# Performance work log

Measured on AMD Instinct MI355X. Metric: run time of the kernel, lower is better.

## Reference

```python
import jax, jax.numpy as jnp
import numpy as np

D = 768        # embed_dim
P = 16         # patch_size
DEPTH = 12
FF = 3072      # dim_feedforward = 4*D
NUM_CLASSES = 100
EPS = 1e-5     # nn.LayerNorm default


def _ln(x, g, b):
    m = jnp.mean(x, axis=-1, keepdims=True)
    v = jnp.mean((x - m) ** 2, axis=-1, keepdims=True)
    return (x - m) / jnp.sqrt(v + EPS) * g + b


def setup_inputs() -> dict:
    key = jax.random.key(0)
    ks = jax.random.split(key, 24)
    f32 = jnp.float32
    inp = {
        'x': jax.random.normal(ks[0], (32, 3, 224, 224), dtype=f32),
        # patch embed conv: [C_in, P, P, D] layout for einsum
        'patch_w': jax.random.normal(ks[1], (3, P, P, D), dtype=f32) * 0.02,
        'patch_b': jnp.zeros((D,), f32),
        'cls_token': jax.random.normal(ks[2], (1, 1, D), dtype=f32) * 0.02,
        'pos_embed': jax.random.normal(ks[3], (1, 197, D), dtype=f32) * 0.02,
        # stacked per-layer params; Linear stored as [in, out]
        'Wq': jax.random.normal(ks[4], (DEPTH, D, D), dtype=f32) * 0.02,
        'bq': jnp.zeros((DEPTH, D), f32),
        'Wk': jax.random.normal(ks[5], (DEPTH, D, D), dtype=f32) * 0.02,
        'bk': jnp.zeros((DEPTH, D), f32),
        'Wv': jax.random.normal(ks[6], (DEPTH, D, D), dtype=f32) * 0.02,
        'bv': jnp.zeros((DEPTH, D), f32),
        'W1': jax.random.normal(ks[7], (DEPTH, D, FF), dtype=f32) * 0.02,
        'b1': jnp.zeros((DEPTH, FF), f32),
        'W2': jax.random.normal(ks[8], (DEPTH, FF, D), dtype=f32) * 0.02,
        'b2': jnp.zeros((DEPTH, D), f32),
        'ln1_g': jnp.ones((DEPTH, D), f32),
        'ln1_b': jnp.zeros((DEPTH, D), f32),
        'ln2_g': jnp.ones((DEPTH, D), f32),
        'ln2_b': jnp.zeros((DEPTH, D), f32),
        'lnf_g': jnp.ones((D,), f32),
        'lnf_b': jnp.zeros((D,), f32),
        'head_w': jax.random.normal(ks[9], (D, NUM_CLASSES), dtype=f32) * 0.02,
        'head_b': jnp.zeros((NUM_CLASSES,), f32),
    }
    return inp


def reference(x, patch_w, patch_b, cls_token, pos_embed,
              Wq, bq, Wk, bk, Wv, bv, W1, b1, W2, b2,
              ln1_g, ln1_b, ln2_g, ln2_b, lnf_g, lnf_b,
              head_w, head_b):
    B = x.shape[0]
    Hp = x.shape[2] // P  # 14
    # patch embed: Conv2d(k=16, s=16) == non-overlapping patch projection
    xp = x.reshape(B, 3, Hp, P, Hp, P)
    tok = jnp.einsum('bchpwq,cpqd->bhwd', xp, patch_w).reshape(B, Hp * Hp, D) + patch_b
    tok = jnp.concatenate([jnp.broadcast_to(cls_token, (B, 1, D)), tok], axis=1)
    tok = tok + pos_embed  # [B, 197, D]
    N = tok.shape[1]
    # gumbel noise for F.gumbel_softmax(tau=1, hard=False), one sample per layer
    gnoise = jax.random.gumbel(jax.random.key(1), (DEPTH, B, N, N), dtype=tok.dtype)
    inv_sqrt_d = 1.0 / jnp.sqrt(jnp.asarray(D, tok.dtype))

    def step(src, p):
        (wq, bq_, wk, bk_, wv, bv_, w1, b1_, w2, b2_,
         g1, be1, g2, be2, gn) = p
        Q = src @ wq + bq_
        K = src @ wk + bk_
        V = src @ wv + bv_
        scores = jnp.einsum('bnd,bmd->bnm', Q, K) * inv_sqrt_d
        attn = jax.nn.softmax(scores + gn, axis=-1) @ V
        src = _ln(src + attn, g1, be1)          # note: out_linear unused in source
        ff = jax.nn.gelu(src @ w1 + b1_, approximate=False) @ w2 + b2_
        src = _ln(src + ff, g2, be2)
        return src, None

    xs = (Wq, bq, Wk, bk, Wv, bv, W1, b1, W2, b2,
          ln1_g, ln1_b, ln2_g, ln2_b, gnoise)
    tok, _ = jax.lax.scan(step, tok, xs)
    tok = _ln(tok, lnf_g, lnf_b)
    cls = tok[:, 0]
    return cls @ head_w + head_b
```

## Files before the change

### kernel.cpp

```cpp
#include <hip/hip_runtime.h>
#include <hip/hip_bf16.h>
#include <math.h>


namespace {
constexpr int DIM    = 768;
constexpr int FF_DIM = 3072;
constexpr int QKVN   = 2304;
constexpr int NTOK   = 197;
constexpr int NBATCH = 32;
constexpr int NLAYER = 12;
constexpr int ROWS   = NBATCH * NTOK;
constexpr int NPATCH = 196;
constexpr int PROWS  = NBATCH * NPATCH;
constexpr int KVPAD  = 256;
constexpr float LN_EPS = 1e-5f;
}

typedef __attribute__((ext_vector_type(8))) __bf16 bf16x8;
typedef __attribute__((ext_vector_type(4))) float  f32x4;

__device__ __forceinline__ unsigned rotl32(unsigned v, int d) {
  return (v << d) | (v >> (32 - d));
}

__device__ __forceinline__ float gumbel_noise(unsigned idx) {
  const unsigned ks0 = 0u, ks1 = 1u, ks2 = 0x1BD11BDBu;
  unsigned x0 = 0u + ks0;
  unsigned x1 = idx + ks1;
#define TFR(r) { x0 += x1; x1 = rotl32(x1, (r)); x1 ^= x0; }
  TFR(13) TFR(15) TFR(26) TFR(6)   x0 += ks1; x1 += ks2 + 1u;
  TFR(17) TFR(29) TFR(16) TFR(24)  x0 += ks2; x1 += ks0 + 2u;
  TFR(13) TFR(15) TFR(26) TFR(6)   x0 += ks0; x1 += ks1 + 3u;
  TFR(17) TFR(29) TFR(16) TFR(24)  x0 += ks1; x1 += ks2 + 4u;
  TFR(13) TFR(15) TFR(26) TFR(6)   x0 += ks2; x1 += ks0 + 5u;
#undef TFR
  unsigned bits = x0 ^ x1;
  float f = __uint_as_float((bits >> 9) | 0x3f800000u) - 1.0f;
  const float tiny = 1.17549435e-38f;
  float u = fmaxf(tiny, f + tiny);
  return -logf(-logf(u));
}

__device__ __forceinline__ float block_reduce_sum(float val, float* red) {
  int tid = threadIdx.x;
  red[tid] = val; __syncthreads();
  for (int off = 128; off > 0; off >>= 1) {
    if (tid < off) red[tid] += red[tid + off];
    __syncthreads();
  }
  float r = red[0];
  __syncthreads();
  return r;
}

__device__ __forceinline__ float block_reduce_max(float val, float* red) {
  int tid = threadIdx.x;
  red[tid] = val; __syncthreads();
  for (int off = 128; off > 0; off >>= 1) {
    if (tid < off) red[tid] = fmaxf(red[tid], red[tid + off]);
    __syncthreads();
  }
  float r = red[0];
  __syncthreads();
  return r;
}

__device__ __forceinline__ void async_copy16(const void* g, void* l) {
  __builtin_amdgcn_global_load_lds(
      (const __attribute__((address_space(1))) unsigned*)g,
      (__attribute__((address_space(3))) unsigned*)l, 16, 0, 0);
}

__device__ __forceinline__ int xcd_swizzle(int id, int nwg) {
  const int q = nwg >> 3, r = nwg & 7;
  const int xcd = id & 7, pos = id >> 3;
  return (xcd < r ? xcd * (q + 1) : r * (q + 1) + (xcd - r) * q) + pos;
}

template<int STORE, bool GELU>
__global__ void mm_nt(
    const __hip_bfloat16* __restrict__ A, long sA, int lda,
    const __hip_bfloat16* __restrict__ B, long sB, int ldb,
    void* __restrict__ Cv, long sC, int ldc,
    int M, int N, int K, const float* __restrict__ bias) {
  __shared__ __hip_bfloat16 As[128 * 64];
  __shared__ __hip_bfloat16 Bs[128 * 64];
  const int bz = blockIdx.y;
  A += (long)bz * sA;
  B += (long)bz * sB;
  const int tilesN = (N + 127) >> 7;
  const int id = xcd_swizzle(blockIdx.x, gridDim.x);
  const int row0 = (id / tilesN) * 128, col0 = (id % tilesN) * 128;

  const int tid = threadIdx.x, lane = tid & 63, wid = tid >> 6;
  const int wr = (wid >> 1) * 64, wc = (wid & 1) * 64;
  const int fr = lane & 15;
  const int kh = lane >> 4;
  const int fsw = fr & 7;
  f32x4 acc[4][4] = {};

  const int elem = wid * 512 + lane * 8;

  for (int k0 = 0; k0 < K; k0 += 64) {
    #pragma unroll
    for (int c = 0; c < 4; c++) {
      const int e = c * 2048 + elem;
      const int r = e >> 6;
      const int slot = (e >> 3) & 7;
      const int ksw = ((slot ^ (r & 7)) << 3);
      async_copy16(A + (long)(row0 + r) * lda + k0 + ksw,
                   (char*)As + c * 4096 + wid * 1024);
    }
    #pragma unroll
    for (int c = 0; c < 4; c++) {
      const int e = c * 2048 + elem;
      const int r = e >> 6;
      const int slot = (e >> 3) & 7;
      const int ksw = ((slot ^ (r & 7)) << 3);
      async_copy16(B + (long)(col0 + r) * ldb + k0 + ksw,
                   (char*)Bs + c * 4096 + wid * 1024);
    }
    __syncthreads();
    #pragma unroll
    for (int ks = 0; ks < 2; ks++) {
      bf16x8 a[4], b[4];
      #pragma unroll
      for (int i = 0; i < 4; i++) {
        const int row = wr + i * 16 + fr;
        const int sl  = ((ks << 2) | kh) ^ fsw;
        a[i] = *(const bf16x8*)((const char*)As + row * 128 + (sl << 4));
      }
      #pragma unroll
      for (int j = 0; j < 4; j++) {
        const int row = wc + j * 16 + fr;
        const int sl  = ((ks << 2) | kh) ^ fsw;
        b[j] = *(const bf16x8*)((const char*)Bs + row * 128 + (sl << 4));
      }
      #pragma unroll
      for (int i = 0; i < 4; i++)
        #pragma unroll
        for (int j = 0; j < 4; j++)
          acc[i][j] = __builtin_amdgcn_mfma_f32_16x16x32_bf16(
              a[i], b[j], acc[i][j], 0, 0, 0);
    }
    __syncthreads();
  }

  #pragma unroll
  for (int i = 0; i < 4; i++) {
    #pragma unroll
    for (int j = 0; j < 4; j++) {
      #pragma unroll
      for (int t = 0; t < 4; t++) {
        const int r  = row0 + wr + i * 16 + kh * 4 + t;
        const int cc = col0 + wc + j * 16 + fr;
        if (r < M && cc < N) {
          float v = acc[i][j][t];
          if (bias) v += bias[cc];
          if (GELU) v = 0.5f * v * (1.0f + erff(v * 0.70710678118654752f));
          if (STORE == 0)
            ((float*)Cv)[(long)bz * sC + (long)r * ldc + cc] = v;
          else
            ((__hip_bfloat16*)Cv)[(long)bz * sC + (long)r * ldc + cc] =
                __float2bfloat16(v);
        }
      }
    }
  }
}

__global__ void transpose_bf16_kernel(const float* __restrict__ W,
                                      __hip_bfloat16* __restrict__ Wt,
                                      int K, int N) {
  __shared__ float t[32][33];
  const int k0 = blockIdx.x * 32, n0 = blockIdx.y * 32;
  const int tx = threadIdx.x & 31, ty = threadIdx.x >> 5;
  #pragma unroll
  for (int i = 0; i < 32; i += 8)
    t[ty + i][tx] = W[(long)(k0 + ty + i) * N + n0 + tx];
  __syncthreads();
  #pragma unroll
  for (int i = 0; i < 32; i += 8)
    Wt[(long)(n0 + ty + i) * K + k0 + tx] = __float2bfloat16(t[tx][ty + i]);
}

__global__ void wtrans_kernel(const float* __restrict__ Wq,
                              const float* __restrict__ Wk,
                              const float* __restrict__ Wv,
                              const float* __restrict__ W1,
                              const float* __restrict__ W2,
                              __hip_bfloat16* __restrict__ wqkv_t,
                              __hip_bfloat16* __restrict__ w1_t,
                              __hip_bfloat16* __restrict__ w2_t,
                              long sq, long s1, long s2) {
  __shared__ float t[64][65];
  const int l = blockIdx.y;
  Wq += (long)l * DIM * DIM;  Wk += (long)l * DIM * DIM;
  Wv += (long)l * DIM * DIM;
  W1 += (long)l * DIM * FF_DIM;  W2 += (long)l * FF_DIM * DIM;
  wqkv_t += (long)l * sq;  w1_t += (long)l * s1;  w2_t += (long)l * s2;

  const int id = blockIdx.x;
  const float* W; __hip_bfloat16* O; int K, N, k0, n0;
  if (id < 432) {
    const int m = id / 144, tt = id % 144;
    W = (m == 0) ? Wq : (m == 1) ? Wk : Wv;
    O = wqkv_t + (long)m * DIM * DIM;
    K = DIM; N = DIM; k0 = (tt / 12) * 64; n0 = (tt % 12) * 64;
  } else if (id < 1008) {
    const int tt = id - 432;
    W = W1; O = w1_t;
    K = DIM; N = FF_DIM; k0 = (tt / 48) * 64; n0 = (tt % 48) * 64;
  } else {
    const int tt = id - 1008;
    W = W2; O = w2_t;
    K = FF_DIM; N = DIM; k0 = (tt / 12) * 64; n0 = (tt % 12) * 64;
  }
  const int tx = threadIdx.x & 63, ty = threadIdx.x >> 6;
  #pragma unroll
  for (int i = 0; i < 16; i++) {
    const int r = ty + i * 4;
    t[r][tx] = W[(long)(k0 + r) * N + n0 + tx];
  }
  __syncthreads();
  #pragma unroll
  for (int i = 0; i < 16; i++) {
    const int r = ty + i * 4;
    O[(long)(n0 + r) * K + k0 + tx] = __float2bfloat16(t[tx][r]);
  }
}

__global__ void build_qkv_bias(const float* __restrict__ bq,
                               const float* __restrict__ bk,
                               const float* __restrict__ bv,
                               float* __restrict__ o) {
  const int l = blockIdx.x;
  for (int d = threadIdx.x; d < DIM; d += 256) {
    o[l * QKVN + d]           = bq[l * DIM + d];
    o[l * QKVN + DIM + d]     = bk[l * DIM + d];
    o[l * QKVN + 2 * DIM + d] = bv[l * DIM + d];
  }
}

__global__ void vtrans_kernel(const __hip_bfloat16* __restrict__ qkv,
                              __hip_bfloat16* __restrict__ vt) {
  __shared__ __hip_bfloat16 s[64][68];
  const int b = blockIdx.z;
  const int t0 = blockIdx.x * 64;
  const int d0 = blockIdx.y * 64;
  const int tx = threadIdx.x & 63, ty = threadIdx.x >> 6;
  for (int i = ty; i < 64; i += 4) {
    const int t = t0 + i;
    __hip_bfloat16 v = __float2bfloat16(0.f);
    if (t < NTOK) v = qkv[(long)(b * NTOK + t) * QKVN + 2 * DIM + d0 + tx];
    s[i][tx] = v;
  }
  __syncthreads();
  for (int i = ty; i < 64; i += 4)
    vt[((long)b * DIM + d0 + i) * KVPAD + t0 + tx] = s[tx][i];
}

__global__ void im2col_kernel(const float* __restrict__ x,
                              __hip_bfloat16* __restrict__ col) {
  const int p = blockIdx.x;
  const int b = p / NPATCH, pi = p % NPATCH;
  const int h = pi / 14, w = pi % 14;
  for (int e = threadIdx.x; e < DIM; e += 256) {
    const int c = e >> 8, r = e & 255, pp = r >> 4, q = r & 15;
    col[(long)p * DIM + e] = __float2bfloat16(
        x[(((long)b * 3 + c) * 224 + h * 16 + pp) * 224 + w * 16 + q]);
  }
}

__global__ void assemble_kernel(const float* __restrict__ tmp,
                                const float* __restrict__ cls,
                                const float* __restrict__ pos,
                                float* __restrict__ tok,
                                __hip_bfloat16* __restrict__ tok_bf) {
  const int row = blockIdx.x;
  const int b = row / NTOK, n = row % NTOK;
  for (int d = threadIdx.x; d < DIM; d += 256) {
    float v = (n == 0) ? cls[d] : tmp[(long)(b * NPATCH + n - 1) * DIM + d];
    v += pos[n * DIM + d];
    tok[(long)row * DIM + d] = v;
    tok_bf[(long)row * DIM + d] = __float2bfloat16(v);
  }
}

__global__ void softmax_kernel(const float* __restrict__ sc,
                               __hip_bfloat16* __restrict__ P, int layer) {
  __shared__ float red[256];
  const int row = blockIdx.x;
  const int b = row / NTOK, n = row % NTOK;
  const int tid = threadIdx.x;
  const long base = (long)row * NTOK;
  const float inv_sqrt_d = 0.036084391824351615f;

  float x = -INFINITY;
  if (tid < NTOK) {
    const unsigned idx =
        ((((unsigned)layer * NBATCH + b) * NTOK + n) * NTOK) + tid;
    x = sc[base + tid] * inv_sqrt_d + gumbel_noise(idx);
  }
  const float mx = block_reduce_max(x, red);
  float ex = (tid < NTOK) ? expf(x - mx) : 0.f;
  const float s = block_reduce_sum(ex, red);
  const float pv = (tid < NTOK) ? ex / s : 0.f;
  P[(long)row * KVPAD + tid] = __float2bfloat16(pv);
}

__global__ void add_ln_kernel(float* __restrict__ tok,
                              __hip_bfloat16* __restrict__ tok_bf,
                              const float* __restrict__ res,
                              const float* __restrict__ res2,
                              const float* __restrict__ rbias,
                              const float* __restrict__ g,
                              const float* __restrict__ beta) {
  __shared__ float red[256];
  const int row = blockIdx.x;
  const int tid = threadIdx.x;
  const long base = (long)row * DIM;
  float v[3];
  float s = 0.f;
  #pragma unroll
  for (int i = 0; i < 3; i++) {
    const int d = tid + (i << 8);
    float r = tok[base + d] + res[base + d];
    if (res2)  r += res2[base + d];
    if (rbias) r += rbias[d];
    v[i] = r;
    s += r;
  }
  const float mean = block_reduce_sum(s, red) * (1.0f / DIM);
  float s2 = 0.f;
  #pragma unroll
  for (int i = 0; i < 3; i++) { const float dd = v[i] - mean; s2 += dd * dd; }
  const float var = block_reduce_sum(s2, red) * (1.0f / DIM);
  const float inv = 1.0f / sqrtf(var + LN_EPS);
  #pragma unroll
  for (int i = 0; i < 3; i++) {
    const int d = tid + (i << 8);
    const float o = (v[i] - mean) * inv * g[d] + beta[d];
    tok[base + d] = o;
    tok_bf[base + d] = __float2bfloat16(o);
  }
}

__global__ void head_kernel(const float* __restrict__ tok,
                            const float* __restrict__ g,
                            const float* __restrict__ beta,
                            const float* __restrict__ hw,
                            const float* __restrict__ hb,
                            float* __restrict__ out) {
  __shared__ float red[256];
  __shared__ float xn[DIM];
  const int b = blockIdx.x;
  const int tid = threadIdx.x;
  const float* xr = tok + (long)b * NTOK * DIM;
  float v[3];
  float s = 0.f;
  #pragma unroll
  for (int i = 0; i < 3; i++) { v[i] = xr[tid + (i << 8)]; s += v[i]; }
  const float mean = block_reduce_sum(s, red) * (1.0f / DIM);
  float s2 = 0.f;
  #pragma unroll
  for (int i = 0; i < 3; i++) { const float dd = v[i] - mean; s2 += dd * dd; }
  const float var = block_reduce_sum(s2, red) * (1.0f / DIM);
  const float inv = 1.0f / sqrtf(var + LN_EPS);
  #pragma unroll
  for (int i = 0; i < 3; i++) {
    const int d = tid + (i << 8);
    xn[d] = (v[i] - mean) * inv * g[d] + beta[d];
  }
  __syncthreads();
  for (int c = tid; c < 100; c += 256) {
    float acc = hb[c];
    for (int d = 0; d < DIM; d++) acc += xn[d] * hw[d * 100 + c];
    out[b * 100 + c] = acc;
  }
}

extern "C" void kernel_launch(void* const* d_in, const int* in_sizes, int n_in,
                              void* d_out, int out_size, void* d_ws, size_t ws_size,
                              hipStream_t stream) {
  const float* x        = (const float*)d_in[0];
  const float* patch_w  = (const float*)d_in[1];
  const float* patch_b  = (const float*)d_in[2];
  const float* cls_tok  = (const float*)d_in[3];
  const float* pos_emb  = (const float*)d_in[4];
  const float* Wq       = (const float*)d_in[5];
  const float* bq       = (const float*)d_in[6];
  const float* Wk       = (const float*)d_in[7];
  const float* bk       = (const float*)d_in[8];
  const float* Wv       = (const float*)d_in[9];
  const float* bv       = (const float*)d_in[10];
  const float* W1       = (const float*)d_in[11];
  const float* b1       = (const float*)d_in[12];
  const float* W2       = (const float*)d_in[13];
  const float* b2       = (const float*)d_in[14];
  const float* ln1_g    = (const float*)d_in[15];
  const float* ln1_b    = (const float*)d_in[16];
  const float* ln2_g    = (const float*)d_in[17];
  const float* ln2_b    = (const float*)d_in[18];
  const float* lnf_g    = (const float*)d_in[19];
  const float* lnf_b    = (const float*)d_in[20];
  const float* head_w   = (const float*)d_in[21];
  const float* head_b   = (const float*)d_in[22];
  float* out = (float*)d_out;

  const long WQKV = (long)QKVN * DIM;
  const long W1SZ = (long)FF_DIM * DIM;
  const long W2SZ = (long)DIM * FF_DIM;
  const long WLAYER = WQKV + W1SZ + W2SZ;

  const long F32N = 3L * 6400 * DIM + (long)NLAYER * QKVN;
  const long BF16FIX = 6400L * DIM + 6400L * FF_DIM +
                       (long)NBATCH * DIM * KVPAD + 6400L * KVPAD +
                       (long)DIM * DIM;
  const size_t need12 = (size_t)F32N * 4 + (size_t)(BF16FIX + 12 * WLAYER) * 2;
  const bool hoist = ws_size >= need12;
  const int NW = hoist ? NLAYER : 1;

  float* fb = (float*)d_ws;
  long fo = 0;
  float* tok      = fb + fo; fo += 6400L * DIM;
  float* b4       = fb + fo; fo += 6400L * DIM;
  float* b4b      = fb + fo; fo += 6400L * DIM;
  float* bias_all = fb + fo; fo += (long)NLAYER * QKVN;
  __hip_bfloat16* hbuf = (__hip_bfloat16*)(fb + fo);
  long ho = 0;
  __hip_bfloat16* tok_bf = hbuf + ho; ho += 6400L * DIM;
  __hip_bfloat16* qkv    = hbuf + ho;
  __hip_bfloat16* ffout  = hbuf + ho; ho += 6400L * FF_DIM;
  float* scbuf = (float*)(qkv + 6400L * QKVN);
  __hip_bfloat16* vt     = hbuf + ho; ho += (long)NBATCH * DIM * KVPAD;
  __hip_bfloat16* Pb     = hbuf + ho; ho += 6400L * KVPAD;
  __hip_bfloat16* pw_t   = hbuf + ho; ho += (long)DIM * DIM;
  __hip_bfloat16* wqkv_t = hbuf + ho; ho += (long)NW * WQKV;
  __hip_bfloat16* w1_t   = hbuf + ho; ho += (long)NW * W1SZ;
  __hip_bfloat16* w2_t   = hbuf + ho; ho += (long)NW * W2SZ;

  const long DD = (long)DIM * DIM;
  const long QKVSTRIDE = (long)NTOK * QKVN;
  const long TOKSTRIDE = (long)NTOK * DIM;
  const long SCSTRIDE  = (long)NTOK * NTOK;
  const long VTSTRIDE  = (long)DIM * KVPAD;
  const long PSTRIDE   = (long)NTOK * KVPAD;

  build_qkv_bias<<<NLAYER, 256, 0, stream>>>(bq, bk, bv, bias_all);

  if (hoist) {
    wtrans_kernel<<<dim3(1584, NLAYER), 256, 0, stream>>>(
        Wq, Wk, Wv, W1, W2, wqkv_t, w1_t, w2_t, WQKV, W1SZ, W2SZ);
  }

  im2col_kernel<<<PROWS, 256, 0, stream>>>(x, ffout);
  transpose_bf16_kernel<<<dim3(DIM / 32, DIM / 32), 256, 0, stream>>>(
      patch_w, pw_t, DIM, DIM);
  mm_nt<0, false><<<dim3(49 * 6, 1), 256, 0, stream>>>(
      ffout, 0, DIM, pw_t, 0, DIM, b4, 0, DIM, PROWS, DIM, DIM, patch_b);
  assemble_kernel<<<ROWS, 256, 0, stream>>>(b4, cls_tok, pos_emb, tok, tok_bf);

  for (int l = 0; l < NLAYER; l++) {
    __hip_bfloat16* wqkv_l = wqkv_t + (hoist ? (long)l * WQKV : 0);
    __hip_bfloat16* w1_l   = w1_t   + (hoist ? (long)l * W1SZ : 0);
    __hip_bfloat16* w2_l   = w2_t   + (hoist ? (long)l * W2SZ : 0);
    if (!hoist) {
      wtrans_kernel<<<dim3(1584, 1), 256, 0, stream>>>(
          Wq + l * DD, Wk + l * DD, Wv + l * DD,
          W1 + (long)l * DIM * FF_DIM, W2 + (long)l * FF_DIM * DIM,
          wqkv_l, w1_l, w2_l, 0, 0, 0);
    }

    mm_nt<1, false><<<dim3(50 * (QKVN / 128), 1), 256, 0, stream>>>(
        tok_bf, 0, DIM, wqkv_l, 0, DIM, qkv, 0, QKVN,
        ROWS, QKVN, DIM, bias_all + l * QKVN);

    vtrans_kernel<<<dim3(KVPAD / 64, DIM / 64, NBATCH), 256, 0, stream>>>(qkv, vt);

    mm_nt<0, false><<<dim3(2 * 2, NBATCH), 256, 0, stream>>>(
        qkv, QKVSTRIDE, QKVN, qkv + DIM, QKVSTRIDE, QKVN, scbuf, SCSTRIDE, NTOK,
        NTOK, NTOK, DIM, nullptr);

    softmax_kernel<<<ROWS, 256, 0, stream>>>(scbuf, Pb, l);

    mm_nt<0, false><<<dim3(2 * (DIM / 128), NBATCH), 256, 0, stream>>>(
        Pb, PSTRIDE, KVPAD, vt, VTSTRIDE, KVPAD, b4, TOKSTRIDE, DIM,
        NTOK, DIM, KVPAD, nullptr);

    add_ln_kernel<<<ROWS, 256, 0, stream>>>(tok, tok_bf, b4, nullptr, nullptr,
        ln1_g + l * DIM, ln1_b + l * DIM);

    mm_nt<1, true><<<dim3(50 * (FF_DIM / 128), 1), 256, 0, stream>>>(
        tok_bf, 0, DIM, w1_l, 0, DIM, ffout, 0, FF_DIM,
        ROWS, FF_DIM, DIM, b1 + l * FF_DIM);

    mm_nt<0, false><<<dim3(50 * (DIM / 128), 2), 256, 0, stream>>>(
        ffout, 1536, FF_DIM, w2_l, 1536, FF_DIM,
        b4, 6400L * DIM, DIM, ROWS, DIM, 1536, nullptr);

    add_ln_kernel<<<ROWS, 256, 0, stream>>>(tok, tok_bf, b4, b4b, b2 + l * DIM,
        ln2_g + l * DIM, ln2_b + l * DIM);
  }

  head_kernel<<<NBATCH, 256, 0, stream>>>(tok, lnf_g, lnf_b, head_w, head_b, out);
}
```

Baseline: 2.956 ms.

## Add 256x256-tile double-buffered GEMM for QKV and FFN1 projections

Adds a new bf16 MFMA GEMM kernel that uses 256x256 output tiles, 512 threads, swizzled shared memory and double-buffered async copies. It is used for the QKV projection and the first FFN matmul, replacing the 128-tile kernel. The larger tile raises data reuse per block and cuts global and LDS traffic, but it uses 128 KB of LDS and many accumulator registers, which may limit occupancy. It also leaves a wave-quantization tail on the 25-row-tile grid. Separately, the weight transpose now loads with float4 vectors.

```diff
diff --git a/kernel.cpp b/kernel.cpp
--- a/kernel.cpp
+++ b/kernel.cpp
@@ -170,6 +170,94 @@
   }
 }
 
+template<int STORE, bool GELU>
+__global__ __launch_bounds__(512, 2) void mm256(
+    const __hip_bfloat16* __restrict__ A, int lda,
+    const __hip_bfloat16* __restrict__ B, int ldb,
+    void* __restrict__ Cv, int ldc,
+    int M, int N, int K, const float* __restrict__ bias) {
+  __shared__ __hip_bfloat16 As[2][256 * 64];
+  __shared__ __hip_bfloat16 Bs[2][256 * 64];
+  const int tilesN = N >> 8;
+  const int id = xcd_swizzle(blockIdx.x, gridDim.x);
+  const int row0 = (id / tilesN) * 256, col0 = (id % tilesN) * 256;
+
+  const int tid = threadIdx.x, lane = tid & 63, wid = tid >> 6;
+  const int wm = wid >> 2, wn = wid & 3;
+  const int fr = lane & 15;
+  const int kh = lane >> 4;
+  const int fsw = fr & 7;
+  f32x4 acc[8][4] = {};
+
+  const int ebase = wid * 2048 + lane * 8;
+
+  auto stage = [&](int buf, int k0) {
+    #pragma unroll
+    for (int c = 0; c < 4; c++) {
+      const int e = ebase + c * 512;
+      const int r = e >> 6;
+      const int slot = (e >> 3) & 7;
+      const int ksw = ((slot ^ (r & 7)) << 3);
+      async_copy16(A + (long)(row0 + r) * lda + k0 + ksw,
+                   (char*)&As[buf][0] + wid * 4096 + c * 1024);
+      async_copy16(B + (long)(col0 + r) * ldb + k0 + ksw,
+                   (char*)&Bs[buf][0] + wid * 4096 + c * 1024);
+    }
+  };
+
+  const int nt = K >> 6;
+  stage(0, 0);
+  __syncthreads();
+  int cur = 0;
+  for (int t = 0; t < nt; ++t) {
+    if (t + 1 < nt) stage(cur ^ 1, (t + 1) << 6);
+    #pragma unroll
+    for (int ks = 0; ks < 2; ks++) {
+      bf16x8 a[8], b[4];
+      const int sl = ((ks << 2) | kh) ^ fsw;
+      #pragma unroll
+      for (int i = 0; i < 8; i++) {
+        const int row = wm * 128 + i * 16 + fr;
+        a[i] = *(const bf16x8*)((const char*)&As[cur][0] + row * 128 + (sl << 4));
+      }
+      #pragma unroll
+      for (int j = 0; j < 4; j++) {
+        const int row = wn * 64 + j * 16 + fr;
+        b[j] = *(const bf16x8*)((const char*)&Bs[cur][0] + row * 128 + (sl << 4));
+      }
+      #pragma unroll
+      for (int i = 0; i < 8; i++)
+        #pragma unroll
+        for (int j = 0; j < 4; j++)
+          acc[i][j] = __builtin_amdgcn_mfma_f32_16x16x32_bf16(
+              a[i], b[j], acc[i][j], 0, 0, 0);
+    }
+    __syncthreads();
+    cur ^= 1;
+  }
+
+  #pragma unroll
+  for (int i = 0; i < 8; i++) {
+    #pragma unroll
+    for (int j = 0; j < 4; j++) {
+      #pragma unroll
+      for (int t = 0; t < 4; t++) {
+        const int r  = row0 + wm * 128 + i * 16 + kh * 4 + t;
+        const int cc = col0 + wn * 64 + j * 16 + fr;
+        if (r < M) {
+          float v = acc[i][j][t];
+          if (bias) v += bias[cc];
+          if (GELU) v = 0.5f * v * (1.0f + erff(v * 0.70710678118654752f));
+          if (STORE == 0)
+            ((float*)Cv)[(long)r * ldc + cc] = v;
+          else
+            ((__hip_bfloat16*)Cv)[(long)r * ldc + cc] = __float2bfloat16(v);
+        }
+      }
+    }
+  }
+}
+
 __global__ void transpose_bf16_kernel(const float* __restrict__ W,
                                       __hip_bfloat16* __restrict__ Wt,
                                       int K, int N) {
@@ -217,13 +305,16 @@
     W = W2; O = w2_t;
     K = FF_DIM; N = DIM; k0 = (tt / 12) * 64; n0 = (tt % 12) * 64;
   }
+  const int c4 = (threadIdx.x & 15) * 4;
+  const int ry = threadIdx.x >> 4;
+  #pragma unroll
+  for (int p = 0; p < 4; p++) {
+    const int r = p * 16 + ry;
+    const float4 v = *(const float4*)&W[(long)(k0 + r) * N + n0 + c4];
+    t[r][c4] = v.x; t[r][c4 + 1] = v.y; t[r][c4 + 2] = v.z; t[r][c4 + 3] = v.w;
+  }
+  __syncthreads();
   const int tx = threadIdx.x & 63, ty = threadIdx.x >> 6;
-  #pragma unroll
-  for (int i = 0; i < 16; i++) {
-    const int r = ty + i * 4;
-    t[r][tx] = W[(long)(k0 + r) * N + n0 + tx];
-  }
-  __syncthreads();
   #pragma unroll
   for (int i = 0; i < 16; i++) {
     const int r = ty + i * 4;
@@ -473,8 +564,8 @@
           wqkv_l, w1_l, w2_l, 0, 0, 0);
     }
 
-    mm_nt<1, false><<<dim3(50 * (QKVN / 128), 1), 256, 0, stream>>>(
-        tok_bf, 0, DIM, wqkv_l, 0, DIM, qkv, 0, QKVN,
+    mm256<1, false><<<25 * (QKVN / 256), 512, 0, stream>>>(
+        tok_bf, DIM, wqkv_l, DIM, qkv, QKVN,
         ROWS, QKVN, DIM, bias_all + l * QKVN);
 
     vtrans_kernel<<<dim3(KVPAD / 64, DIM / 64, NBATCH), 256, 0, stream>>>(qkv, vt);
@@ -492,8 +583,8 @@
     add_ln_kernel<<<ROWS, 256, 0, stream>>>(tok, tok_bf, b4, nullptr, nullptr,
         ln1_g + l * DIM, ln1_b + l * DIM);
 
-    mm_nt<1, true><<<dim3(50 * (FF_DIM / 128), 1), 256, 0, stream>>>(
-        tok_bf, 0, DIM, w1_l, 0, DIM, ffout, 0, FF_DIM,
+    mm256<1, true><<<25 * (FF_DIM / 256), 512, 0, stream>>>(
+        tok_bf, DIM, w1_l, DIM, ffout, FF_DIM,
         ROWS, FF_DIM, DIM, b1 + l * FF_DIM);
 
     mm_nt<0, false><<<dim3(50 * (DIM / 128), 2), 256, 0, stream>>>(
```

New measurement: 4.128 ms. 1.4x slower.
